# Kernel tuning notes

Measured on AMD Instinct MI355X. Metric: run time of the kernel, lower is better.

## Reference

```python
import jax, jax.numpy as jnp
import numpy as np

N = 20000      # nodes
E = 640000     # edges (avg degree 32)
F = 6          # feature_dim
D = 128        # weight_dim
L = 3          # lstm num_layers
DEPTH = 10     # extra iterations after initial call


def setup_inputs() -> dict:
    key = jax.random.key(0)
    ks = jax.random.split(key, 10)
    s = 0.05
    return {
        "features": jax.random.normal(ks[0], (N, F), jnp.float32),
        "src": jax.random.randint(ks[1], (E,), 0, N),
        "dst": jax.random.randint(ks[2], (E,), 0, N),
        "W_in": jax.random.normal(ks[3], (F, D), jnp.float32) * s,
        "b_in": jnp.zeros((D,), jnp.float32),
        "Wih0": jax.random.normal(ks[4], (4 * D, 2 * D), jnp.float32) * s,   # layer 0: input = concat(h_in, feat)
        "Wih_rest": jax.random.normal(ks[5], (2, 4 * D, D), jnp.float32) * s,  # layers 1,2
        "Whh": jax.random.normal(ks[6], (L, 4 * D, D), jnp.float32) * s,
        "bih": jnp.zeros((L, 4 * D), jnp.float32),
        "bhh": jnp.zeros((L, 4 * D), jnp.float32),
        "W_out": jax.random.normal(ks[7], (D, 1), jnp.float32) * s,
        "b_out": jnp.zeros((1,), jnp.float32),
    }


def _lstm_cell(x, h, c, Wih, Whh, b):
    # PyTorch gate order: i, f, g, o
    gates = x @ Wih.T + h @ Whh.T + b              # [N, 4D]
    i, f, g, o = jnp.split(gates, 4, axis=-1)
    i = jax.nn.sigmoid(i)
    f = jax.nn.sigmoid(f)
    o = jax.nn.sigmoid(o)
    g = jnp.tanh(g)
    c_new = f * c + i * g
    h_new = o * jnp.tanh(c_new)
    return h_new, c_new


def reference(features, src, dst, W_in, b_in, Wih0, Wih_rest, Whh, bih, bhh, W_out, b_out):
    n = features.shape[0]
    b = bih + bhh                                   # [L, 4D]

    def agg(x):
        # DGL update_all(copy_src, mean): mean over incoming edges (src -> dst)
        s = jax.ops.segment_sum(x[src], dst, num_segments=n)
        deg = jax.ops.segment_sum(jnp.ones((src.shape[0],), x.dtype), dst, num_segments=n)
        return jnp.where(deg[:, None] > 0, s / jnp.maximum(deg, 1.0)[:, None], 0.0)

    feat = jax.nn.relu(features @ W_in + b_in)      # [N, D]
    h = jnp.zeros((L, n, D), features.dtype)
    c = jnp.zeros((L, n, D), features.dtype)

    def step(carry, _):
        feat, h, c = carry
        x0 = jnp.concatenate([agg(feat), feat], axis=-1)   # [N, 2D]
        h0, c0 = _lstm_cell(x0, h[0], c[0], Wih0, Whh[0], b[0])
        h1, c1 = _lstm_cell(h0, h[1], c[1], Wih_rest[0], Whh[1], b[1])
        h2, c2 = _lstm_cell(h1, h[2], c[2], Wih_rest[1], Whh[2], b[2])
        return (h2, jnp.stack([h0, h1, h2]), jnp.stack([c0, c1, c2])), None

    # initial call + depth extra iterations, all structurally identical
    (feat, h, c), _ = jax.lax.scan(step, (feat, h, c), None, length=1 + DEPTH)
    return h[-1] @ W_out + b_out                    # [N, 1]
```

## Files before the change

### kernel.cpp

```cpp
#include <hip/hip_runtime.h>
#include <math.h>

typedef _Float16 f16;
typedef __attribute__((ext_vector_type(8))) _Float16 half8;
typedef __attribute__((ext_vector_type(4))) float float4v;

__device__ __forceinline__ float fast_sigmoid(float x) { return 1.0f / (1.0f + __expf(-x)); }
__device__ __forceinline__ float fast_tanh(float x) {
    float a = fabsf(x);
    float e = __expf(-2.0f * a);
    float t = (1.0f - e) / (1.0f + e);
    return copysignf(t, x);
}

__device__ __forceinline__ void async_copy16(const void* gsrc, void* ldst) {
    __builtin_amdgcn_global_load_lds(
        (const __attribute__((address_space(1))) void*)gsrc,
        (__attribute__((address_space(3))) void*)ldst,
        16, 0, 0);
}

__global__ void packb_kernel(const float* __restrict__ Wih, int Kih,
                             const float* __restrict__ Whh, int K,
                             const float* __restrict__ bih, const float* __restrict__ bhh,
                             f16* __restrict__ Bp, float* __restrict__ bp) {
    int t = blockIdx.x * blockDim.x + threadIdx.x;
    if (t >= (K << 9)) return;
    int colp = t / K;
    int k = t - colp * K;
    int dg = colp >> 6, q = (colp >> 4) & 3, dl = colp & 15;
    int j = q * 128 + dg * 16 + dl;
    float v = (k < Kih) ? Wih[j * Kih + k] : Whh[j * (K - Kih) + (k - Kih)];
    Bp[t] = (f16)v;
    if (k == 0) bp[colp] = bih[j] + bhh[j];
}

__global__ void feat0_kernel(const float* __restrict__ features, const float* __restrict__ W_in,
                             const float* __restrict__ b_in, f16* __restrict__ feat, int n) {
    int t = blockIdx.x * blockDim.x + threadIdx.x;
    if (t >= n * 128) return;
    int node = t >> 7;
    int d = t & 127;
    float s = b_in[d];
#pragma unroll
    for (int k = 0; k < 6; ++k) s += features[node * 6 + k] * W_in[k * 128 + d];
    feat[t] = (f16)fmaxf(s, 0.0f);
}

__global__ void hist_kernel(const int* __restrict__ dst, int* __restrict__ cnt, int e) {
    int t = blockIdx.x * blockDim.x + threadIdx.x;
    if (t < e) atomicAdd(&cnt[dst[t]], 1);
}

__global__ void scan_kernel(const int* __restrict__ cnt, int* __restrict__ off,
                            int* __restrict__ cur, float* __restrict__ recip, int n) {
    __shared__ int wsum[16];
    __shared__ int stot;
    int t = threadIdx.x;
    int lane = t & 63, wv = t >> 6;
    int R = 0;
    int rounds = (n + 1023) >> 10;
    for (int i = 0; i < rounds; ++i) {
        int idx = (i << 10) + t;
        int v = (idx < n) ? cnt[idx] : 0;
        int s = v;
#pragma unroll
        for (int o = 1; o < 64; o <<= 1) {
            int u = __shfl_up(s, o, 64);
            if (lane >= o) s += u;
        }
        if (lane == 63) wsum[wv] = s;
        __syncthreads();
        if (t == 0) {
            int a = 0;
#pragma unroll
            for (int j = 0; j < 16; ++j) { int x = wsum[j]; wsum[j] = a; a += x; }
            stot = a;
        }
        __syncthreads();
        int excl = R + wsum[wv] + s - v;
        if (idx < n) {
            off[idx] = excl; cur[idx] = excl;
            recip[idx] = (v > 0) ? 1.0f / (float)v : 0.0f;
        }
        R += stot;
        __syncthreads();
    }
    if (t == 0) off[n] = R;
}

__global__ void scatter_kernel(const int* __restrict__ src, const int* __restrict__ dst,
                               int* __restrict__ cur, int* __restrict__ esrc, int e) {
    int t = blockIdx.x * blockDim.x + threadIdx.x;
    if (t >= e) return;
    int d = dst[t];
    int p = atomicAdd(&cur[d], 1);
    esrc[p] = src[t];
}

__global__ __launch_bounds__(256, 6) void agg_kernel(
    const f16* __restrict__ feat, const int* __restrict__ off,
    const int* __restrict__ esrc, const float* __restrict__ recip,
    f16* __restrict__ agg, int n) {
    int slot = threadIdx.x >> 4;
    int lane = threadIdx.x & 15;
    int v = blockIdx.x * 16 + slot;
    if (v >= n) return;
    int e0 = off[v], e1 = off[v + 1];
    float a[8];
#pragma unroll
    for (int j = 0; j < 8; ++j) a[j] = 0.0f;
    int e = e0;
    for (; e + 8 <= e1; e += 8) {
        int ss[8];
#pragma unroll
        for (int u = 0; u < 8; ++u) ss[u] = esrc[e + u];
        half8 vv[8];
#pragma unroll
        for (int u = 0; u < 8; ++u)
            vv[u] = *(const half8*)&feat[(size_t)ss[u] * 128 + lane * 8];
#pragma unroll
        for (int u = 0; u < 8; ++u)
#pragma unroll
            for (int j = 0; j < 8; ++j) a[j] += (float)vv[u][j];
    }
    for (; e < e1; ++e) {
        int s = esrc[e];
        half8 v0 = *(const half8*)&feat[(size_t)s * 128 + lane * 8];
#pragma unroll
        for (int j = 0; j < 8; ++j) a[j] += (float)v0[j];
    }
    float r = recip[v];
    half8 o;
#pragma unroll
    for (int j = 0; j < 8; ++j) o[j] = (f16)(a[j] * r);
    *(half8*)&agg[(size_t)v * 128 + lane * 8] = o;
}

#define BM 64

template <int PARTS>
__global__ __launch_bounds__(256, 3) void gemm_lstm(
    const f16* __restrict__ A0, const f16* __restrict__ A1, const f16* __restrict__ A2,
    const f16* __restrict__ Bp, const float* __restrict__ bp,
    float* __restrict__ c, f16* __restrict__ h_out, int nrows) {
    constexpr int K = PARTS * 128;
    constexpr int NT = PARTS * 4;
    __shared__ f16 As[2][64 * 32];
    __shared__ f16 Bs[2][256 * 32];

    const int tid = threadIdx.x;
    const int w = tid >> 6;
    const int lane = tid & 63;
    const int dl = lane & 15;
    const int quad = lane >> 4;
    const int row0 = blockIdx.x * BM;
    const int cb = blockIdx.y;

    float4v acc[4][4];
#pragma unroll
    for (int q = 0; q < 4; ++q) {
        float b = bp[cb * 256 + w * 64 + q * 16 + dl];
#pragma unroll
        for (int rt = 0; rt < 4; ++rt) {
            acc[rt][q][0] = b; acc[rt][q][1] = b; acc[rt][q][2] = b; acc[rt][q][3] = b;
        }
    }

    const int srow = lane >> 2;
    const int sj = lane & 3;
    const int sg = sj ^ ((srow >> 1) & 3);
    const int rslot = (quad ^ ((dl >> 1) & 3)) << 3;

    auto stage = [&](int kt, int bsel) {
        const f16* Ap = A0;
        const int pi = kt >> 2;
        if (PARTS >= 2 && pi == 1) Ap = A1;
        if (PARTS >= 3 && pi == 2) Ap = A2;
        const int kk = (kt & 3) * 32;
        async_copy16(&Ap[(size_t)(row0 + w * 16 + srow) * 128 + kk + (sg << 3)],
                     (f16*)As[bsel] + w * 512);
        const f16* Bbase = Bp + (size_t)(cb * 256) * K + kt * 32;
#pragma unroll
        for (int i = 0; i < 4; ++i) {
            int m = i * 4 + w;
            async_copy16(&Bbase[(size_t)(m * 16 + srow) * K + (sg << 3)],
                         (f16*)Bs[bsel] + m * 512);
        }
    };

    stage(0, 0);
    __syncthreads();

    for (int kt = 0; kt < NT; ++kt) {
        const int cur = kt & 1;
        if (kt + 1 < NT) stage(kt + 1, cur ^ 1);

        half8 a[4], b[4];
#pragma unroll
        for (int rt = 0; rt < 4; ++rt)
            a[rt] = *(const half8*)&As[cur][(rt * 16 + dl) * 32 + rslot];
#pragma unroll
        for (int q = 0; q < 4; ++q)
            b[q] = *(const half8*)&Bs[cur][((w * 4 + q) * 16 + dl) * 32 + rslot];
#pragma unroll
        for (int rt = 0; rt < 4; ++rt)
#pragma unroll
            for (int q = 0; q < 4; ++q)
                acc[rt][q] = __builtin_amdgcn_mfma_f32_16x16x32_f16(a[rt], b[q], acc[rt][q], 0, 0, 0);

        __syncthreads();
    }

    float* cpriv = c + ((size_t)(blockIdx.x * 2 + cb)) * 4096;
    const int d = cb * 64 + w * 16 + dl;
#pragma unroll
    for (int rt = 0; rt < 4; ++rt) {
        float4v ig = acc[rt][0], fg = acc[rt][1], gg = acc[rt][2], og = acc[rt][3];
        float* cp = cpriv + rt * 1024 + tid * 4;
        float4v cold = *(const float4v*)cp;
        float4v cn;
        float hn[4];
#pragma unroll
        for (int r = 0; r < 4; ++r) {
            float i_ = fast_sigmoid(ig[r]);
            float f_ = fast_sigmoid(fg[r]);
            float g_ = fast_tanh(gg[r]);
            float o_ = fast_sigmoid(og[r]);
            float cv = f_ * cold[r] + i_ * g_;
            cn[r] = cv;
            hn[r] = o_ * fast_tanh(cv);
        }
        *(float4v*)cp = cn;
#pragma unroll
        for (int r = 0; r < 4; ++r) {
            int nr = row0 + rt * 16 + (quad << 2) + r;
            if (nr < nrows) h_out[(size_t)nr * 128 + d] = (f16)hn[r];
        }
    }
}

__global__ void out_kernel(const f16* __restrict__ h2, const float* __restrict__ Wout,
                           const float* __restrict__ bout, float* __restrict__ out) {
    int n = blockIdx.x;
    int l = threadIdx.x;
    float v = (float)h2[(size_t)n * 128 + l] * Wout[l] +
              (float)h2[(size_t)n * 128 + 64 + l] * Wout[64 + l];
#pragma unroll
    for (int o = 32; o > 0; o >>= 1) v += __shfl_down(v, o, 64);
    if (l == 0) out[n] = v + bout[0];
}

extern "C" void kernel_launch(void* const* d_in, const int* in_sizes, int n_in,
                              void* d_out, int out_size, void* d_ws, size_t ws_size,
                              hipStream_t stream) {
    const float* features = (const float*)d_in[0];
    const int*   src      = (const int*)d_in[1];
    const int*   dst      = (const int*)d_in[2];
    const float* W_in     = (const float*)d_in[3];
    const float* b_in     = (const float*)d_in[4];
    const float* Wih0     = (const float*)d_in[5];
    const float* Wih_rest = (const float*)d_in[6];
    const float* Whh      = (const float*)d_in[7];
    const float* bih      = (const float*)d_in[8];
    const float* bhh      = (const float*)d_in[9];
    const float* W_out    = (const float*)d_in[10];
    const float* b_out    = (const float*)d_in[11];
    float* out = (float*)d_out;

    const int N = in_sizes[0] / 6;
    const int E = in_sizes[1];
    const int NP = N + BM;

    char* ws = (char*)d_ws;
    size_t pos = 0;
    auto alloc = [&](size_t bytes) -> void* {
        void* p = ws + pos;
        pos = (pos + bytes + 255) & ~(size_t)255;
        return p;
    };
    const size_t hrow = 128;
    const size_t hbytes = (size_t)NP * hrow * sizeof(f16);
    const size_t cbytes = (size_t)NP * hrow * sizeof(float);
    f16* feath = (f16*)alloc(hbytes);
    f16* aggh  = (f16*)alloc(hbytes);
    f16* hblk  = (f16*)alloc(6 * hbytes);
    f16* hA[3], * hB[3];
    for (int l = 0; l < 3; ++l) {
        hA[l] = hblk + (size_t)l * NP * hrow;
        hB[l] = hblk + (size_t)(l + 3) * NP * hrow;
    }
    float* cblk = (float*)alloc(3 * cbytes);
    float* c0 = cblk + 0 * (size_t)NP * hrow;
    float* c1 = cblk + 1 * (size_t)NP * hrow;
    float* c2 = cblk + 2 * (size_t)NP * hrow;
    f16* Bp0 = (f16*)alloc((size_t)512 * 384 * sizeof(f16));
    f16* Bp1 = (f16*)alloc((size_t)512 * 256 * sizeof(f16));
    f16* Bp2 = (f16*)alloc((size_t)512 * 256 * sizeof(f16));
    float* bp0 = (float*)alloc(512 * sizeof(float));
    float* bp1 = (float*)alloc(512 * sizeof(float));
    float* bp2 = (float*)alloc(512 * sizeof(float));
    int*   cnt   = (int*)alloc((size_t)N * 4);
    int*   offs  = (int*)alloc((size_t)(N + 1) * 4);
    int*   cur   = (int*)alloc((size_t)N * 4);
    int*   esrc  = (int*)alloc((size_t)E * 4);
    float* recip = (float*)alloc((size_t)N * 4);

    hipMemsetAsync(hblk, 0, 6 * hbytes, stream);
    hipMemsetAsync(cblk, 0, 3 * cbytes, stream);
    hipMemsetAsync(cnt, 0, (size_t)N * 4, stream);

    packb_kernel<<<(512 * 384 + 255) / 256, 256, 0, stream>>>(
        Wih0, 256, Whh, 384, bih, bhh, Bp0, bp0);
    packb_kernel<<<(512 * 256 + 255) / 256, 256, 0, stream>>>(
        Wih_rest, 128, Whh + 512 * 128, 256, bih + 512, bhh + 512, Bp1, bp1);
    packb_kernel<<<(512 * 256 + 255) / 256, 256, 0, stream>>>(
        Wih_rest + 512 * 128, 128, Whh + 2 * 512 * 128, 256, bih + 1024, bhh + 1024, Bp2, bp2);

    feat0_kernel<<<(N * 128 + 255) / 256, 256, 0, stream>>>(features, W_in, b_in, feath, N);
    hist_kernel<<<(E + 255) / 256, 256, 0, stream>>>(dst, cnt, E);
    scan_kernel<<<1, 1024, 0, stream>>>(cnt, offs, cur, recip, N);
    scatter_kernel<<<(E + 255) / 256, 256, 0, stream>>>(src, dst, cur, esrc, E);

    const dim3 ggrid((N + BM - 1) / BM, 2, 1);
    const int gagg = (N + 15) / 16;
    const f16* featcur = feath;
    f16 *r0 = hA[0], *r1 = hA[1], *r2 = hA[2];
    f16 *w0 = hB[0], *w1 = hB[1], *w2 = hB[2];
    for (int step = 0; step < 11; ++step) {
        agg_kernel<<<gagg, 256, 0, stream>>>(featcur, offs, esrc, recip, aggh, N);
        gemm_lstm<3><<<ggrid, 256, 0, stream>>>(aggh, featcur, r0, Bp0, bp0, c0, w0, N);
        gemm_lstm<2><<<ggrid, 256, 0, stream>>>(w0, r1, nullptr, Bp1, bp1, c1, w1, N);
        gemm_lstm<2><<<ggrid, 256, 0, stream>>>(w1, r2, nullptr, Bp2, bp2, c2, w2, N);
        featcur = w2;
        f16* t;
        t = r0; r0 = w0; w0 = t;
        t = r1; r1 = w1; w1 = t;
        t = r2; r2 = w2; w2 = t;
    }
    out_kernel<<<N, 64, 0, stream>>>((const f16*)featcur, W_out, b_out, out);
}
```

Baseline: 1.080 ms.

## Load GEMM operands directly from global memory instead of LDS double-buffering

Removes the LDS staging (async global_load_lds double buffer and barriers) from the LSTM gate GEMM. Each lane now loads its A and B MFMA fragments straight from global memory with a fully unrolled K loop, relying on L1/L2 for reuse. To make out-of-range row reads safe, the padded tail rows of the feature and aggregate buffers are zeroed. This trades barrier and LDS overhead for more global/cache traffic, because each wave re-reads A rows that other waves also load, and the per-lane access pattern is less coalesced.

Result: slower. 1.443 ms (+33.5%).

```diff
diff --git a/kernel.cpp b/kernel.cpp
--- a/kernel.cpp
+++ b/kernel.cpp
@@ -11,13 +11,6 @@
     float e = __expf(-2.0f * a);
     float t = (1.0f - e) / (1.0f + e);
     return copysignf(t, x);
-}
-
-__device__ __forceinline__ void async_copy16(const void* gsrc, void* ldst) {
-    __builtin_amdgcn_global_load_lds(
-        (const __attribute__((address_space(1))) void*)gsrc,
-        (__attribute__((address_space(3))) void*)ldst,
-        16, 0, 0);
 }
 
 __global__ void packb_kernel(const float* __restrict__ Wih, int Kih,
@@ -146,8 +139,6 @@
     float* __restrict__ c, f16* __restrict__ h_out, int nrows) {
     constexpr int K = PARTS * 128;
     constexpr int NT = PARTS * 4;
-    __shared__ f16 As[2][64 * 32];
-    __shared__ f16 Bs[2][256 * 32];
 
     const int tid = threadIdx.x;
     const int w = tid >> 6;
@@ -167,49 +158,35 @@
         }
     }
 
-    const int srow = lane >> 2;
-    const int sj = lane & 3;
-    const int sg = sj ^ ((srow >> 1) & 3);
-    const int rslot = (quad ^ ((dl >> 1) & 3)) << 3;
-
-    auto stage = [&](int kt, int bsel) {
-        const f16* Ap = A0;
+    const int kq = quad * 8;
+    size_t abase[4];
+#pragma unroll
+    for (int rt = 0; rt < 4; ++rt)
+        abase[rt] = (size_t)(row0 + rt * 16 + dl) * 128 + kq;
+    const f16* bcol[4];
+#pragma unroll
+    for (int q = 0; q < 4; ++q)
+        bcol[q] = Bp + (size_t)(cb * 256 + w * 64 + q * 16 + dl) * K + kq;
+
+#pragma unroll
+    for (int kt = 0; kt < NT; ++kt) {
         const int pi = kt >> 2;
-        if (PARTS >= 2 && pi == 1) Ap = A1;
-        if (PARTS >= 3 && pi == 2) Ap = A2;
+        const f16* Ap = (PARTS >= 3 && pi == 2) ? A2
+                      : (PARTS >= 2 && pi == 1) ? A1 : A0;
         const int kk = (kt & 3) * 32;
-        async_copy16(&Ap[(size_t)(row0 + w * 16 + srow) * 128 + kk + (sg << 3)],
-                     (f16*)As[bsel] + w * 512);
-        const f16* Bbase = Bp + (size_t)(cb * 256) * K + kt * 32;
-#pragma unroll
-        for (int i = 0; i < 4; ++i) {
-            int m = i * 4 + w;
-            async_copy16(&Bbase[(size_t)(m * 16 + srow) * K + (sg << 3)],
-                         (f16*)Bs[bsel] + m * 512);
-        }
-    };
-
-    stage(0, 0);
-    __syncthreads();
-
-    for (int kt = 0; kt < NT; ++kt) {
-        const int cur = kt & 1;
-        if (kt + 1 < NT) stage(kt + 1, cur ^ 1);
 
         half8 a[4], b[4];
 #pragma unroll
         for (int rt = 0; rt < 4; ++rt)
-            a[rt] = *(const half8*)&As[cur][(rt * 16 + dl) * 32 + rslot];
+            a[rt] = *(const half8*)&Ap[abase[rt] + kk];
 #pragma unroll
         for (int q = 0; q < 4; ++q)
-            b[q] = *(const half8*)&Bs[cur][((w * 4 + q) * 16 + dl) * 32 + rslot];
+            b[q] = *(const half8*)&bcol[q][kt * 32];
 #pragma unroll
         for (int rt = 0; rt < 4; ++rt)
 #pragma unroll
             for (int q = 0; q < 4; ++q)
                 acc[rt][q] = __builtin_amdgcn_mfma_f32_16x16x32_f16(a[rt], b[q], acc[rt][q], 0, 0, 0);
-
-        __syncthreads();
     }
 
     float* cpriv = c + ((size_t)(blockIdx.x * 2 + cb)) * 4096;
@@ -309,6 +286,8 @@
     hipMemsetAsync(hblk, 0, 6 * hbytes, stream);
     hipMemsetAsync(cblk, 0, 3 * cbytes, stream);
     hipMemsetAsync(cnt, 0, (size_t)N * 4, stream);
+    hipMemsetAsync(feath + (size_t)N * hrow, 0, (size_t)(NP - N) * hrow * sizeof(f16), stream);
+    hipMemsetAsync(aggh + (size_t)N * hrow, 0, (size_t)(NP - N) * hrow * sizeof(f16), stream);
 
     packb_kernel<<<(512 * 384 + 255) / 256, 256, 0, stream>>>(
         Wih0, 256, Whh, 384, bih, bhh, Bp0, bp0);
```

## Software-pipeline neighbor gather and skip zero-state work in first LSTM step

Applied to the files above, without the earlier changes.

The aggregation kernel now double-buffers index loads and feature gathers across 8-edge batches, so the next batch's loads are in flight while the current batch accumulates. Occupancy bounds are lowered to make room for the extra registers. A FIRST template variant of the LSTM GEMM skips the recurrent-weight K tiles and the old cell-state read on step zero, because h and c start at zero. This removes the large h/c memsets, replacing them with padding-only memsets, which assumes the skipped tiles never read uninitialised h buffers.

Measured after the change: 1.087 ms. No clear change (+0.6%).

```diff
diff --git a/kernel.cpp b/kernel.cpp
--- a/kernel.cpp
+++ b/kernel.cpp
@@ -98,38 +98,77 @@
     esrc[p] = src[t];
 }
 
-__global__ __launch_bounds__(256, 6) void agg_kernel(
+__global__ __launch_bounds__(256, 4) void agg_kernel(
     const f16* __restrict__ feat, const int* __restrict__ off,
     const int* __restrict__ esrc, const float* __restrict__ recip,
     f16* __restrict__ agg, int n) {
-    int slot = threadIdx.x >> 4;
     int lane = threadIdx.x & 15;
-    int v = blockIdx.x * 16 + slot;
+    int v = blockIdx.x * 16 + (threadIdx.x >> 4);
     if (v >= n) return;
-    int e0 = off[v], e1 = off[v + 1];
+    const int e0 = off[v], e1 = off[v + 1];
     float a[8];
 #pragma unroll
     for (int j = 0; j < 8; ++j) a[j] = 0.0f;
+
+    const int nb = (e1 - e0) >> 3;
     int e = e0;
-    for (; e + 8 <= e1; e += 8) {
-        int ss[8];
-#pragma unroll
-        for (int u = 0; u < 8; ++u) ss[u] = esrc[e + u];
-        half8 vv[8];
-#pragma unroll
-        for (int u = 0; u < 8; ++u)
-            vv[u] = *(const half8*)&feat[(size_t)ss[u] * 128 + lane * 8];
-#pragma unroll
-        for (int u = 0; u < 8; ++u)
-#pragma unroll
-            for (int j = 0; j < 8; ++j) a[j] += (float)vv[u][j];
-    }
-    for (; e < e1; ++e) {
-        int s = esrc[e];
-        half8 v0 = *(const half8*)&feat[(size_t)s * 128 + lane * 8];
+
+#define GATHER(dst_, s_) \
+    _Pragma("unroll") for (int u = 0; u < 8; ++u) \
+        dst_[u] = *(const half8*)&feat[(size_t)s_[u] * 128 + lane * 8];
+#define ACC(v_) \
+    _Pragma("unroll") for (int u = 0; u < 8; ++u) \
+        _Pragma("unroll") for (int j = 0; j < 8; ++j) a[j] += (float)v_[u][j];
+#define LDIDX(s_, base_) \
+    _Pragma("unroll") for (int u = 0; u < 8; ++u) s_[u] = esrc[(base_) + u];
+
+    if (nb >= 2) {
+        int sA[8], sB[8];
+        half8 vA[8], vB[8];
+        LDIDX(sA, e);
+        LDIDX(sB, e + 8);
+        e += 16;
+        GATHER(vA, sA);
+        int b = nb - 2;
+        while (b >= 2) {
+            LDIDX(sA, e);
+            GATHER(vB, sB);
+            ACC(vA);
+            LDIDX(sB, e + 8);
+            GATHER(vA, sA);
+            ACC(vB);
+            e += 16;
+            b -= 2;
+        }
+        if (b == 1) {
+            int sN[8];
+            LDIDX(sN, e);
+            GATHER(vB, sB);
+            ACC(vA);
+            GATHER(vA, sN);
+            ACC(vB);
+            ACC(vA);
+        } else {
+            GATHER(vB, sB);
+            ACC(vA);
+            ACC(vB);
+        }
+    } else if (nb == 1) {
+        int sA[8];
+        half8 vA[8];
+        LDIDX(sA, e);
+        GATHER(vA, sA);
+        ACC(vA);
+    }
+    for (int t = e0 + (nb << 3); t < e1; ++t) {
+        half8 v0 = *(const half8*)&feat[(size_t)esrc[t] * 128 + lane * 8];
 #pragma unroll
         for (int j = 0; j < 8; ++j) a[j] += (float)v0[j];
     }
+#undef GATHER
+#undef ACC
+#undef LDIDX
+
     float r = recip[v];
     half8 o;
 #pragma unroll
@@ -139,13 +178,13 @@
 
 #define BM 64
 
-template <int PARTS>
+template <int PARTS, bool FIRST>
 __global__ __launch_bounds__(256, 3) void gemm_lstm(
     const f16* __restrict__ A0, const f16* __restrict__ A1, const f16* __restrict__ A2,
     const f16* __restrict__ Bp, const float* __restrict__ bp,
     float* __restrict__ c, f16* __restrict__ h_out, int nrows) {
     constexpr int K = PARTS * 128;
-    constexpr int NT = PARTS * 4;
+    constexpr int NT = FIRST ? (PARTS - 1) * 4 : PARTS * 4;
     __shared__ f16 As[2][64 * 32];
     __shared__ f16 Bs[2][256 * 32];
 
@@ -218,7 +257,12 @@
     for (int rt = 0; rt < 4; ++rt) {
         float4v ig = acc[rt][0], fg = acc[rt][1], gg = acc[rt][2], og = acc[rt][3];
         float* cp = cpriv + rt * 1024 + tid * 4;
-        float4v cold = *(const float4v*)cp;
+        float4v cold;
+        if (FIRST) {
+            cold[0] = 0.0f; cold[1] = 0.0f; cold[2] = 0.0f; cold[3] = 0.0f;
+        } else {
+            cold = *(const float4v*)cp;
+        }
         float4v cn;
         float hn[4];
 #pragma unroll
@@ -306,9 +350,9 @@
     int*   esrc  = (int*)alloc((size_t)E * 4);
     float* recip = (float*)alloc((size_t)N * 4);
 
-    hipMemsetAsync(hblk, 0, 6 * hbytes, stream);
-    hipMemsetAsync(cblk, 0, 3 * cbytes, stream);
     hipMemsetAsync(cnt, 0, (size_t)N * 4, stream);
+    hipMemsetAsync(feath + (size_t)N * hrow, 0, (size_t)(NP - N) * hrow * sizeof(f16), stream);
+    hipMemsetAsync(aggh + (size_t)N * hrow, 0, (size_t)(NP - N) * hrow * sizeof(f16), stream);
 
     packb_kernel<<<(512 * 384 + 255) / 256, 256, 0, stream>>>(
         Wih0, 256, Whh, 384, bih, bhh, Bp0, bp0);
@@ -329,9 +373,15 @@
     f16 *w0 = hB[0], *w1 = hB[1], *w2 = hB[2];
     for (int step = 0; step < 11; ++step) {
         agg_kernel<<<gagg, 256, 0, stream>>>(featcur, offs, esrc, recip, aggh, N);
-        gemm_lstm<3><<<ggrid, 256, 0, stream>>>(aggh, featcur, r0, Bp0, bp0, c0, w0, N);
-        gemm_lstm<2><<<ggrid, 256, 0, stream>>>(w0, r1, nullptr, Bp1, bp1, c1, w1, N);
-        gemm_lstm<2><<<ggrid, 256, 0, stream>>>(w1, r2, nullptr, Bp2, bp2, c2, w2, N);
+        if (step == 0) {
+            gemm_lstm<3, true ><<<ggrid, 256, 0, stream>>>(aggh, featcur, r0, Bp0, bp0, c0, w0, N);
+            gemm_lstm<2, true ><<<ggrid, 256, 0, stream>>>(w0, r1, nullptr, Bp1, bp1, c1, w1, N);
+            gemm_lstm<2, true ><<<ggrid, 256, 0, stream>>>(w1, r2, nullptr, Bp2, bp2, c2, w2, N);
+        } else {
+            gemm_lstm<3, false><<<ggrid, 256, 0, stream>>>(aggh, featcur, r0, Bp0, bp0, c0, w0, N);
+            gemm_lstm<2, false><<<ggrid, 256, 0, stream>>>(w0, r1, nullptr, Bp1, bp1, c1, w1, N);
+            gemm_lstm<2, false><<<ggrid, 256, 0, stream>>>(w1, r2, nullptr, Bp2, bp2, c2, w2, N);
+        }
         featcur = w2;
         f16* t;
         t = r0; r0 = w0; w0 = t;
```
